# Performance work log

Measured on AMD Instinct MI355X. Metric: run time of the kernel, lower is better.

## Reference

```python
import jax, jax.numpy as jnp
import numpy as np

R = 3            # corr_radius
KK = 2 * R + 1   # 7
K = KK * KK      # 49 support points
LEVELS = 4       # corr_levels


def _offsets():
    # matches get_support_points: meshgrid over [-r, r] applied to (x, y)
    d = jnp.arange(-R, R + 1, dtype=jnp.float32)
    ox, oy = jnp.meshgrid(d, d, indexing='ij')
    return jnp.stack([ox, oy], -1).reshape(K, 2)


def _bilinear(fmap_flat, fidx, x, y):
    """Bilinear sample with zero padding (grid_sample align_corners=True semantics
    for pixel-space coords). fmap_flat: (F,H,W,D); fidx int (...); x,y float (...).
    Returns (..., D)."""
    Hs, Ws = fmap_flat.shape[1], fmap_flat.shape[2]
    x0 = jnp.floor(x); y0 = jnp.floor(y)
    tx = x - x0; ty = y - y0

    def tap(xi, yi, w):
        valid = (xi >= 0) & (xi <= Ws - 1) & (yi >= 0) & (yi <= Hs - 1)
        xc = jnp.clip(xi, 0, Ws - 1).astype(jnp.int32)
        yc = jnp.clip(yi, 0, Hs - 1).astype(jnp.int32)
        return fmap_flat[fidx, yc, xc] * (w * valid)[..., None]

    return (tap(x0, y0, (1 - tx) * (1 - ty)) + tap(x0 + 1, y0, tx * (1 - ty))
            + tap(x0, y0 + 1, (1 - tx) * ty) + tap(x0 + 1, y0 + 1, tx * ty))


def reference(fmaps, coords, queried_coords, queried_frames, w1, b1, w2, b2):
    """Multi-scale correlation-volume pipeline of CoTrackerThreeOffline:
    L2-normalize fmaps, build avg-pool pyramid, sample 7x7 track-support feats
    at query frames, sample 7x7 correlation feats at current coords per frame,
    einsum 49x49 corr volume, corr_mlp (2401->384 GELU ->256), concat levels."""
    B, T, D, H, W = fmaps.shape
    N = coords.shape[2]
    fm = jnp.transpose(fmaps, (0, 1, 3, 4, 2))  # (B,T,H,W,D)
    fm = fm / jnp.sqrt(jnp.maximum(jnp.sum(fm * fm, -1, keepdims=True), 1e-12))
    offs = _offsets()
    fidx_t = jnp.arange(B * T).reshape(B, T, 1, 1)          # frame index per (b,t)
    fq = (jnp.arange(B)[:, None] * T + queried_frames)[..., None]  # (B,N,1)
    embs = []
    for lvl in range(LEVELS):
        Hs, Ws = fm.shape[2], fm.shape[3]
        fm_flat = fm.reshape(B * T, Hs, Ws, D)
        # track support features at the query frame (7x7 around query coord)
        qc = queried_coords / (2.0 ** lvl)                   # (B,N,2)
        px = qc[..., 0:1] + offs[:, 0]; py = qc[..., 1:2] + offs[:, 1]  # (B,N,K)
        tf = _bilinear(fm_flat, fq, px, py)                  # (B,N,K,D)
        # correlation features around current coords for every frame
        cl = coords / (2.0 ** lvl)                           # (B,T,N,2)
        cx = cl[..., 0:1] + offs[:, 0]; cy = cl[..., 1:2] + offs[:, 1]  # (B,T,N,K)
        cf = _bilinear(fm_flat, fidx_t, cx, cy)              # (B,T,N,K,D)
        # 49x49 correlation volume then corr_mlp
        vol = jnp.einsum('btnkc,bnlc->btnkl', cf, tf).reshape(B * T * N, K * K)
        emb = jax.nn.gelu(vol @ w1 + b1, approximate=False) @ w2 + b2
        embs.append(emb.reshape(B, T, N, -1))
        if lvl < LEVELS - 1:  # avg_pool2d k=2 s=2
            fm = fm.reshape(B, T, Hs // 2, 2, Ws // 2, 2, D).mean(axis=(3, 5))
    return jnp.concatenate(embs, -1)  # (B,T,N,4*256)


def setup_inputs() -> dict:
    key = jax.random.key(0)
    ks = jax.random.split(key, 6)
    B, T, D, H, W, N = 1, 24, 128, 96, 128, 256
    fmaps = jax.random.normal(ks[0], (B, T, D, H, W), jnp.float32)
    scale_xy = jnp.array([W - 1.0, H - 1.0], jnp.float32)
    queried_coords = jax.random.uniform(ks[1], (B, N, 2), jnp.float32) * scale_xy
    queried_frames = jax.random.randint(ks[2], (B, N), 0, T)
    coords = jax.random.uniform(ks[3], (B, T, N, 2), jnp.float32) * scale_xy
    w1 = jax.random.normal(ks[4], (K * K, 384), jnp.float32) * 0.02
    b1 = jnp.zeros((384,), jnp.float32)
    w2 = jax.random.normal(ks[5], (384, 256), jnp.float32) * 0.02
    b2 = jnp.zeros((256,), jnp.float32)
    return dict(fmaps=fmaps, coords=coords, queried_coords=queried_coords,
                queried_frames=queried_frames, w1=w1, b1=b1, w2=w2, b2=b2)
```

## Files before the change

kernel.cpp:

```cpp
#include <hip/hip_runtime.h>
#include <hip/hip_bf16.h>
#include <stdint.h>

#define T_   24
#define D_   128
#define H_   96
#define W_   128
#define N_   256
#define KP   49
#define K2   3136
#define H1   384
#define OUTC 256
#define MTOT (4 * T_ * N_)

#define PAD  8

typedef __attribute__((ext_vector_type(8))) __bf16 bf16x8;
typedef __attribute__((ext_vector_type(4))) float f32x4;

typedef __attribute__((address_space(3))) unsigned int lds_u32;
typedef const __attribute__((address_space(1))) unsigned int g_u32;
#define GLOAD16(g, l) __builtin_amdgcn_global_load_lds((g_u32*)(g), (lds_u32*)(l), 16, 0, 0)

__device__ inline float bf2f(unsigned short u) {
    union { unsigned int i; float f; } v; v.i = ((unsigned int)u) << 16; return v.f;
}
__device__ inline unsigned short f2bf(float f) {
    union { float f; unsigned int i; } v; v.f = f;
    unsigned int i = v.i;
    return (unsigned short)((i + 0x7FFFu + ((i >> 16) & 1u)) >> 16);
}

__global__ __launch_bounds__(256) void k_padzero(uint4* __restrict__ fm,
                                                 int Hs, int Ws) {
    int PW = Ws + 2 * PAD, PH = Hs + 2 * PAD;
    size_t upf = (size_t)PH * PW * 16;
    size_t total = upf * T_;
    for (size_t idx = (size_t)blockIdx.x * 256 + threadIdx.x; idx < total;
         idx += (size_t)gridDim.x * 256) {
        size_t p = idx >> 4;
        size_t pf = p % ((size_t)PH * PW);
        int y = (int)(pf / PW), x = (int)(pf % PW);
        if (y < PAD || y >= Hs + PAD || x < PAD || x >= Ws + PAD) {
            uint4 z = {0u, 0u, 0u, 0u};
            fm[idx] = z;
        }
    }
}

__global__ __launch_bounds__(256) void k_w1t(const float* __restrict__ w1,
                                             unsigned short* __restrict__ w1t) {
    __shared__ float tile[64][65];
    int bn = blockIdx.x, k = blockIdx.y;
    int tid = threadIdx.x;
    int nl = tid & 63, q = tid >> 6;
#pragma unroll
    for (int i = 0; i < 16; ++i) {
        int l = q * 16 + i;
        float v = (l < KP) ? w1[((size_t)k * KP + l) * H1 + bn * 64 + nl] : 0.f;
        tile[l][nl] = v;
    }
    __syncthreads();
#pragma unroll
    for (int i = 0; i < 16; ++i) {
        int nn = q * 16 + i;
        w1t[(size_t)(bn * 64 + nn) * K2 + k * 64 + nl] = f2bf(tile[nl][nn]);
    }
}
__global__ __launch_bounds__(256) void k_w2t(const float* __restrict__ w2,
                                             unsigned short* __restrict__ w2t) {
    int idx = blockIdx.x * 256 + threadIdx.x;
    if (idx >= OUTC * H1) return;
    int j = idx / H1, k = idx % H1;
    w2t[idx] = f2bf(w2[(size_t)k * OUTC + j]);
}

#define PW0 (W_ + 2 * PAD)
#define FR0 ((size_t)(H_ + 2 * PAD) * PW0 * D_)
__global__ __launch_bounds__(256) void k_normalize(const float* __restrict__ fmaps,
                                                   unsigned short* __restrict__ fm0i) {
    int bid = blockIdx.x;
    int t = bid / H_, h = bid % H_;
    int tid = threadIdx.x;
    __shared__ float tile[64 * 129];
    __shared__ float ssumP[64][4];
    __shared__ float rs[64];
    const float* base = fmaps + (size_t)t * D_ * H_ * W_ + (size_t)h * W_;
    unsigned short* orow = fm0i + (size_t)t * FR0 + (size_t)h * (PW0 * D_);
    for (int wt = 0; wt < 2; ++wt) {
        int wl = tid & 63, dg = tid >> 6;
        float ss = 0.f;
        for (int i = 0; i < 32; ++i) {
            int d = dg * 32 + i;
            float v = base[(size_t)d * (H_ * W_) + wt * 64 + wl];
            tile[wl * 129 + d] = v;
            ss += v * v;
        }
        ssumP[wl][dg] = ss;
        __syncthreads();
        if (tid < 64)
            rs[tid] = rsqrtf(fmaxf(ssumP[tid][0] + ssumP[tid][1] + ssumP[tid][2] + ssumP[tid][3], 1e-12f));
        __syncthreads();
        int c = tid & 63, rg = tid >> 6;
        for (int i = 0; i < 16; ++i) {
            int wll = rg * 16 + i;
            float r = rs[wll];
            float v0 = tile[wll * 129 + c * 2] * r;
            float v1 = tile[wll * 129 + c * 2 + 1] * r;
            *(unsigned int*)(orow + (size_t)(wt * 64 + wll) * D_ + c * 2) =
                (unsigned int)f2bf(v0) | ((unsigned int)f2bf(v1) << 16);
        }
        __syncthreads();
    }
}

__global__ __launch_bounds__(256) void k_pool(const unsigned short* __restrict__ ini,
                                              unsigned short* __restrict__ outi,
                                              int Hs, int Ws) {
    int Ho = Hs >> 1, Wo = Ws >> 1;
    int PWi = Ws + 2 * PAD, PWo = Wo + 2 * PAD;
    size_t FRi = (size_t)(Hs + 2 * PAD) * PWi * D_;
    size_t FRo = (size_t)(Ho + 2 * PAD) * PWo * D_;
    size_t total = (size_t)T_ * Ho * Wo * (D_ / 4);
    size_t idx = (size_t)blockIdx.x * 256 + threadIdx.x;
    if (idx >= total) return;
    int d4 = idx & 31;
    size_t p = idx >> 5;
    int x = (int)(p % Wo); p /= Wo;
    int y = (int)(p % Ho); int t = (int)(p / Ho);
    const unsigned short* b0 = ini + (size_t)t * FRi + ((size_t)(2 * y) * PWi + 2 * x) * D_ + d4 * 4;
    const unsigned short* b1r = b0 + (size_t)PWi * D_;
    float acc[4] = {0.f, 0.f, 0.f, 0.f};
#pragma unroll
    for (int j = 0; j < 2; ++j) {
        const unsigned short* bb = j ? b1r : b0;
#pragma unroll
        for (int i = 0; i < 2; ++i) {
            const unsigned short* q = bb + i * D_;
#pragma unroll
            for (int c = 0; c < 4; ++c) acc[c] += bf2f(q[c]);
        }
    }
    unsigned short* o = outi + (size_t)t * FRo + ((size_t)y * PWo + x) * D_ + d4 * 4;
#pragma unroll
    for (int c = 0; c < 4; ++c) o[c] = f2bf(acc[c] * 0.25f);
}

__device__ inline float2 bilin2p(const unsigned short* __restrict__ fb, int PW,
                                 float px, float py, int lane) {
    float x0f = floorf(px), y0f = floorf(py);
    float tx = px - x0f, ty = py - y0f;
    int x0 = (int)x0f, y0 = (int)y0f;
    float acc0 = 0.f, acc1 = 0.f;
#pragma unroll
    for (int dy = 0; dy < 2; ++dy) {
#pragma unroll
        for (int dx = 0; dx < 2; ++dx) {
            long xi = x0 + dx, yi = y0 + dy;
            float w = (dx ? tx : 1.f - tx) * (dy ? ty : 1.f - ty);
            unsigned int pk = *(const unsigned int*)(fb + (yi * PW + xi) * D_ + lane * 2);
            acc0 += w * bf2f((unsigned short)(pk & 0xffffu));
            acc1 += w * bf2f((unsigned short)(pk >> 16));
        }
    }
    return {acc0, acc1};
}

__global__ __launch_bounds__(256) void k_tf(const unsigned short* __restrict__ f0,
                                            const unsigned short* __restrict__ f1,
                                            const unsigned short* __restrict__ f2,
                                            const unsigned short* __restrict__ f3,
                                            const float* __restrict__ qcoords,
                                            const int* __restrict__ qframes,
                                            unsigned short* __restrict__ tfg) {
    int n = blockIdx.x, lvl = blockIdx.y;
    const unsigned short* fmi = lvl == 0 ? f0 : lvl == 1 ? f1 : lvl == 2 ? f2 : f3;
    int Hs = H_ >> lvl, Ws = W_ >> lvl;
    int PW = Ws + 2 * PAD;
    size_t FR = (size_t)(Hs + 2 * PAD) * PW * D_;
    float inv = 1.0f / (float)(1 << lvl);
    int wid = threadIdx.x >> 6, lane = threadIdx.x & 63;
    int fidx = qframes[n];
    float qx = qcoords[n * 2 + 0] * inv, qy = qcoords[n * 2 + 1] * inv;
    const unsigned short* fb = fmi + (size_t)fidx * FR;
    unsigned short* orow = tfg + ((size_t)lvl * N_ + n) * (64 * D_);
    for (int k = wid; k < 64; k += 4) {
        float2 v = {0.f, 0.f};
        if (k < KP) {
            float px = qx + (float)(k / 7 - 3);
            float py = qy + (float)(k % 7 - 3);
            v = bilin2p(fb, PW, px, py, lane);
        }
        unsigned int pk = (unsigned int)f2bf(v.x) | ((unsigned int)f2bf(v.y) << 16);
        *(unsigned int*)(orow + k * D_ + lane * 2) = pk;
    }
}

__global__ __launch_bounds__(256) void k_cfvol(const unsigned short* __restrict__ f0,
                                               const unsigned short* __restrict__ f1,
                                               const unsigned short* __restrict__ f2,
                                               const unsigned short* __restrict__ f3,
                                               const float* __restrict__ coords,
                                               const unsigned short* __restrict__ tfg,
                                               unsigned short* __restrict__ vol) {
    __shared__ unsigned char tfs[16384];
    __shared__ unsigned char Ps[16384];
    unsigned short* Gs = (unsigned short*)tfs;
    int n = blockIdx.x, t = blockIdx.y, lvl = blockIdx.z;
    const unsigned short* fmi = lvl == 0 ? f0 : lvl == 1 ? f1 : lvl == 2 ? f2 : f3;
    int Hs = H_ >> lvl, Ws = W_ >> lvl;
    int PW = Ws + 2 * PAD;
    size_t FR = (size_t)(Hs + 2 * PAD) * PW * D_;
    float inv = 1.0f / (float)(1 << lvl);
    int tid = threadIdx.x, wid = tid >> 6, lane = tid & 63;
    int l15 = lane & 15, hi = lane >> 4;

    float cx = coords[((size_t)t * N_ + n) * 2 + 0] * inv;
    float cy = coords[((size_t)t * N_ + n) * 2 + 1] * inv;
    float fx = floorf(cx), fy = floorf(cy);
    float tx = cx - fx, ty = cy - fy;
    long bx = (long)(int)fx - 3, by = (long)(int)fy - 3;
    const unsigned short* fb = fmi + (size_t)t * FR;
    const unsigned short* tfn = tfg + ((size_t)lvl * N_ + n) * (64 * D_);
#pragma unroll
    for (int i = 0; i < 4; ++i) {
        int rr = wid * 16 + i * 4 + hi;
        int u = l15 ^ (rr & 7);
        GLOAD16(tfn + rr * 128 + u * 8, tfs + (wid * 4 + i) * 1024);
    }
#pragma unroll
    for (int i = 0; i < 4; ++i) {
        int rr = wid * 16 + i * 4 + hi;
        int u = l15 ^ (rr & 7);
        GLOAD16(fb + ((by + (rr & 7)) * (long)PW + (bx + (rr >> 3))) * D_ + u * 8,
                Ps + (wid * 4 + i) * 1024);
    }
    asm volatile("s_waitcnt vmcnt(0)" ::: "memory");
    __builtin_amdgcn_s_barrier();
    f32x4 acc[4] = {f32x4{0,0,0,0}, f32x4{0,0,0,0}, f32x4{0,0,0,0}, f32x4{0,0,0,0}};
#pragma unroll
    for (int ks = 0; ks < 4; ++ks) {
        int colb = ks * 64 + hi * 16;
        int arow = wid * 16 + l15;
        bf16x8 a = *(const bf16x8*)(Ps + arow * 256 + (colb ^ ((arow & 7) << 4)));
#pragma unroll
        for (int ln = 0; ln < 4; ++ln) {
            int brow = ln * 16 + l15;
            bf16x8 b = *(const bf16x8*)(tfs + brow * 256 + (colb ^ ((brow & 7) << 4)));
            acc[ln] = __builtin_amdgcn_mfma_f32_16x16x32_bf16(a, b, acc[ln], 0, 0, 0);
        }
    }
    __syncthreads();
#pragma unroll
    for (int ln = 0; ln < 4; ++ln)
#pragma unroll
        for (int r = 0; r < 4; ++r)
            Gs[(wid * 16 + hi * 4 + r) * 64 + ln * 16 + l15] = f2bf(acc[ln][r]);
    __syncthreads();
    unsigned int* vrow = (unsigned int*)(vol + (((size_t)lvl * T_ + t) * N_ + n) * K2);
    float w00 = (1.f - tx) * (1.f - ty), w01 = (1.f - tx) * ty;
    float w10 = tx * (1.f - ty), w11 = tx * ty;
    int lh = lane >> 5, ll = lane & 31;
#pragma unroll
    for (int it = 0; it < 7; ++it) {
        int k = it * 8 + wid * 2 + lh;
        if (k < KP) {
            int a0 = k / 7, b0 = k - a0 * 7;
            int g = a0 * 8 + b0;
            const unsigned short* gp = &Gs[g * 64 + ll * 2];
            unsigned int u00 = *(const unsigned int*)(gp);
            unsigned int u01 = *(const unsigned int*)(gp + 64);
            unsigned int u10 = *(const unsigned int*)(gp + 8 * 64);
            unsigned int u11 = *(const unsigned int*)(gp + 9 * 64);
            float r0 = w00 * bf2f((unsigned short)u00) + w01 * bf2f((unsigned short)u01)
                     + w10 * bf2f((unsigned short)u10) + w11 * bf2f((unsigned short)u11);
            float r1 = w00 * bf2f((unsigned short)(u00 >> 16)) + w01 * bf2f((unsigned short)(u01 >> 16))
                     + w10 * bf2f((unsigned short)(u10 >> 16)) + w11 * bf2f((unsigned short)(u11 >> 16));
            vrow[k * 32 + ll] = (unsigned int)f2bf(r0) | ((unsigned int)f2bf(r1) << 16);
        }
    }
}

__global__ __launch_bounds__(256) void k_gemm1(const unsigned short* __restrict__ A,
                                               const unsigned short* __restrict__ Bt,
                                               const float* __restrict__ b1,
                                               unsigned short* __restrict__ Hout) {
    __shared__ unsigned char As[8192];
    __shared__ unsigned char Bs[16384];
    int bid = blockIdx.x;
    int swz = (bid & 7) * 144 + (bid >> 3);
    int bm = swz / 3, bn = swz % 3;
    int tid = threadIdx.x, lane = tid & 63;
    int wid = tid >> 6, wm = wid & 1, wn = wid >> 1;
    int l15 = lane & 15, hi = lane >> 4;
    f32x4 acc[2][4] = {};
    const unsigned short* Abase = A + (size_t)(bm * 64) * K2;
    const unsigned short* Bbase = Bt + (size_t)(bn * 128) * K2;
    for (int kt = 0; kt < K2 / 64; ++kt) {
#pragma unroll
        for (int q = 0; q < 2; ++q) {
            int e = (wid * 2 + q) * 64 + lane;
            int row = e >> 3, su = (e & 7) ^ (row & 7);
            GLOAD16(Abase + (size_t)row * K2 + kt * 64 + su * 8, As + (wid * 2 + q) * 1024);
        }
#pragma unroll
        for (int q = 0; q < 4; ++q) {
            int e = (wid * 4 + q) * 64 + lane;
            int row = e >> 3, su = (e & 7) ^ (row & 7);
            GLOAD16(Bbase + (size_t)row * K2 + kt * 64 + su * 8, Bs + (wid * 4 + q) * 1024);
        }
        __syncthreads();
#pragma unroll
        for (int ks = 0; ks < 2; ++ks) {
            int colb = ks * 64 + hi * 16;
            bf16x8 a[2], b[4];
#pragma unroll
            for (int km = 0; km < 2; ++km) {
                int arow = wm * 32 + km * 16 + l15;
                a[km] = *(const bf16x8*)(As + arow * 128 + (colb ^ ((arow & 7) << 4)));
            }
#pragma unroll
            for (int ln = 0; ln < 4; ++ln) {
                int brow = wn * 64 + ln * 16 + l15;
                b[ln] = *(const bf16x8*)(Bs + brow * 128 + (colb ^ ((brow & 7) << 4)));
            }
#pragma unroll
            for (int km = 0; km < 2; ++km)
#pragma unroll
                for (int ln = 0; ln < 4; ++ln)
                    acc[km][ln] = __builtin_amdgcn_mfma_f32_16x16x32_bf16(a[km], b[ln], acc[km][ln], 0, 0, 0);
        }
        __syncthreads();
    }
#pragma unroll
    for (int km = 0; km < 2; ++km)
#pragma unroll
        for (int ln = 0; ln < 4; ++ln)
#pragma unroll
            for (int r = 0; r < 4; ++r) {
                int row = bm * 64 + wm * 32 + km * 16 + hi * 4 + r;
                int col = bn * 128 + wn * 64 + ln * 16 + l15;
                float x = acc[km][ln][r] + b1[col];
                float g = 0.5f * x * (1.f + erff(x * 0.70710678118654752f));
                Hout[(size_t)row * H1 + col] = f2bf(g);
            }
}

__global__ __launch_bounds__(256) void k_gemm2(const unsigned short* __restrict__ A,
                                               const unsigned short* __restrict__ Bt,
                                               const float* __restrict__ b2,
                                               float* __restrict__ outp) {
    __shared__ unsigned char As[8192];
    __shared__ unsigned char Bs[16384];
    int bid = blockIdx.x;
    int swz = (bid & 7) * 96 + (bid >> 3);
    int bm = swz >> 1, bn = swz & 1;
    int tid = threadIdx.x, lane = tid & 63;
    int wid = tid >> 6, wm = wid & 1, wn = wid >> 1;
    int l15 = lane & 15, hi = lane >> 4;
    f32x4 acc[2][4] = {};
    const unsigned short* Abase = A + (size_t)(bm * 64) * H1;
    const unsigned short* Bbase = Bt + (size_t)(bn * 128) * H1;
    for (int kt = 0; kt < H1 / 64; ++kt) {
#pragma unroll
        for (int q = 0; q < 2; ++q) {
            int e = (wid * 2 + q) * 64 + lane;
            int row = e >> 3, su = (e & 7) ^ (row & 7);
            GLOAD16(Abase + (size_t)row * H1 + kt * 64 + su * 8, As + (wid * 2 + q) * 1024);
        }
#pragma unroll
        for (int q = 0; q < 4; ++q) {
            int e = (wid * 4 + q) * 64 + lane;
            int row = e >> 3, su = (e & 7) ^ (row & 7);
            GLOAD16(Bbase + (size_t)row * H1 + kt * 64 + su * 8, Bs + (wid * 4 + q) * 1024);
        }
        __syncthreads();
#pragma unroll
        for (int ks = 0; ks < 2; ++ks) {
            int colb = ks * 64 + hi * 16;
            bf16x8 a[2], b[4];
#pragma unroll
            for (int km = 0; km < 2; ++km) {
                int arow = wm * 32 + km * 16 + l15;
                a[km] = *(const bf16x8*)(As + arow * 128 + (colb ^ ((arow & 7) << 4)));
            }
#pragma unroll
            for (int ln = 0; ln < 4; ++ln) {
                int brow = wn * 64 + ln * 16 + l15;
                b[ln] = *(const bf16x8*)(Bs + brow * 128 + (colb ^ ((brow & 7) << 4)));
            }
#pragma unroll
            for (int km = 0; km < 2; ++km)
#pragma unroll
                for (int ln = 0; ln < 4; ++ln)
                    acc[km][ln] = __builtin_amdgcn_mfma_f32_16x16x32_bf16(a[km], b[ln], acc[km][ln], 0, 0, 0);
        }
        __syncthreads();
    }
#pragma unroll
    for (int km = 0; km < 2; ++km)
#pragma unroll
        for (int ln = 0; ln < 4; ++ln)
#pragma unroll
            for (int r = 0; r < 4; ++r) {
                int row = bm * 64 + wm * 32 + km * 16 + hi * 4 + r;
                int col = bn * 128 + wn * 64 + ln * 16 + l15;
                int lvl = row / (T_ * N_);
                int r2 = row - lvl * (T_ * N_);
                outp[(size_t)r2 * (4 * OUTC) + lvl * OUTC + col] = acc[km][ln][r] + b2[col];
            }
}

extern "C" void kernel_launch(void* const* d_in, const int* in_sizes, int n_in,
                              void* d_out, int out_size, void* d_ws, size_t ws_size,
                              hipStream_t stream) {
    const float* fmaps   = (const float*)d_in[0];
    const float* coords  = (const float*)d_in[1];
    const float* qcoords = (const float*)d_in[2];
    const int*   qframes = (const int*)d_in[3];
    const float* w1      = (const float*)d_in[4];
    const float* b1      = (const float*)d_in[5];
    const float* w2      = (const float*)d_in[6];
    const float* b2      = (const float*)d_in[7];
    float* outp = (float*)d_out;

    unsigned char* ws = (unsigned char*)d_ws;
    size_t off = 0;
    auto take = [&](size_t bytes) {
        unsigned char* p = ws + off;
        off += (bytes + 255) & ~(size_t)255;
        return p;
    };
    const int Hs[4] = {96, 48, 24, 12}, Wss[4] = {128, 64, 32, 16};
    unsigned short* fmraw[4];
    unsigned short* fmint[4];
    for (int l = 0; l < 4; ++l) {
        int PH = Hs[l] + 2 * PAD, PW = Wss[l] + 2 * PAD;
        fmraw[l] = (unsigned short*)take((size_t)T_ * PH * PW * D_ * 2);
        fmint[l] = fmraw[l] + ((size_t)PAD * PW + PAD) * D_;
    }
    unsigned short* tfg  = (unsigned short*)take((size_t)4 * N_ * 64 * D_ * 2);
    unsigned short* vol  = (unsigned short*)take((size_t)MTOT * K2 * 2);
    unsigned short* hbuf = (unsigned short*)take((size_t)MTOT * H1 * 2);
    unsigned short* w1t  = (unsigned short*)take((size_t)H1 * K2 * 2);
    unsigned short* w2t  = (unsigned short*)take((size_t)OUTC * H1 * 2);

    for (int l = 0; l < 4; ++l)
        hipLaunchKernelGGL(k_padzero, dim3(4096), dim3(256), 0, stream,
                           (uint4*)fmraw[l], Hs[l], Wss[l]);
    hipLaunchKernelGGL(k_w1t, dim3(6, 49), dim3(256), 0, stream, w1, w1t);
    hipLaunchKernelGGL(k_w2t, dim3((OUTC * H1 + 255) / 256), dim3(256), 0, stream, w2, w2t);
    hipLaunchKernelGGL(k_normalize, dim3(T_ * H_), dim3(256), 0, stream, fmaps, fmint[0]);
    hipLaunchKernelGGL(k_pool, dim3((T_ * 48 * 64 * 32 + 255) / 256), dim3(256), 0, stream,
                       fmint[0], fmint[1], 96, 128);
    hipLaunchKernelGGL(k_pool, dim3((T_ * 24 * 32 * 32 + 255) / 256), dim3(256), 0, stream,
                       fmint[1], fmint[2], 48, 64);
    hipLaunchKernelGGL(k_pool, dim3((T_ * 12 * 16 * 32 + 255) / 256), dim3(256), 0, stream,
                       fmint[2], fmint[3], 24, 32);

    hipLaunchKernelGGL(k_tf, dim3(N_, 4), dim3(256), 0, stream,
                       fmint[0], fmint[1], fmint[2], fmint[3], qcoords, qframes, tfg);
    hipLaunchKernelGGL(k_cfvol, dim3(N_, T_, 4), dim3(256), 0, stream,
                       fmint[0], fmint[1], fmint[2], fmint[3], coords, tfg, vol);
    hipLaunchKernelGGL(k_gemm1, dim3(384 * 3), dim3(256), 0, stream, vol, w1t, b1, hbuf);
    hipLaunchKernelGGL(k_gemm2, dim3(384 * 2), dim3(256), 0, stream, hbuf, w2t, b2, outp);
}
```

Baseline: 324.8 us.

## Split-K the first MLP GEMM in two halves with separate bias+GELU reduction kernel

Pads the correlation-volume K dimension from 3136 to 3200 so it divides into two halves, and splits the first MLP GEMM into two K-halves, doubling the block count from 1152 to 2304. Each half writes fp32 partial sums to a new workspace. A separate kernel then sums the two partials, adds the bias, applies GELU and stores bf16. The aim is to fill the GPU better for the long-K GEMM. The cost is roughly 28 MB of extra fp32 partial traffic, one more launch, and a small amount of padded zero work.

New measurement: 354.3 us. 1.09x slower.

```diff
diff --git a/kernel.cpp b/kernel.cpp
--- a/kernel.cpp
+++ b/kernel.cpp
@@ -8,7 +8,7 @@
 #define W_   128
 #define N_   256
 #define KP   49
-#define K2   3136
+#define K2   3200
 #define H1   384
 #define OUTC 256
 #define MTOT (4 * T_ * N_)
@@ -57,7 +57,7 @@
 #pragma unroll
     for (int i = 0; i < 16; ++i) {
         int l = q * 16 + i;
-        float v = (l < KP) ? w1[((size_t)k * KP + l) * H1 + bn * 64 + nl] : 0.f;
+        float v = (k < KP && l < KP) ? w1[((size_t)k * KP + l) * H1 + bn * 64 + nl] : 0.f;
         tile[l][nl] = v;
     }
     __syncthreads();
@@ -279,24 +279,26 @@
             vrow[k * 32 + ll] = (unsigned int)f2bf(r0) | ((unsigned int)f2bf(r1) << 16);
         }
     }
-}
-
-__global__ __launch_bounds__(256) void k_gemm1(const unsigned short* __restrict__ A,
-                                               const unsigned short* __restrict__ Bt,
-                                               const float* __restrict__ b1,
-                                               unsigned short* __restrict__ Hout) {
+    if (tid < 32) vrow[1568 + tid] = 0u;
+}
+
+__global__ __launch_bounds__(256) void k_gemm1a(const unsigned short* __restrict__ A,
+                                                const unsigned short* __restrict__ Bt,
+                                                float* __restrict__ part) {
     __shared__ unsigned char As[8192];
     __shared__ unsigned char Bs[16384];
     int bid = blockIdx.x;
-    int swz = (bid & 7) * 144 + (bid >> 3);
-    int bm = swz / 3, bn = swz % 3;
+    int swz = (bid & 7) * 288 + (bid >> 3);
+    int tile = swz >> 1, kh = swz & 1;
+    int bm = tile / 3, bn = tile % 3;
     int tid = threadIdx.x, lane = tid & 63;
     int wid = tid >> 6, wm = wid & 1, wn = wid >> 1;
     int l15 = lane & 15, hi = lane >> 4;
     f32x4 acc[2][4] = {};
     const unsigned short* Abase = A + (size_t)(bm * 64) * K2;
     const unsigned short* Bbase = Bt + (size_t)(bn * 128) * K2;
-    for (int kt = 0; kt < K2 / 64; ++kt) {
+    const int KH = (K2 / 64) / 2;
+    for (int kt = kh * KH; kt < kh * KH + KH; ++kt) {
 #pragma unroll
         for (int q = 0; q < 2; ++q) {
             int e = (wid * 2 + q) * 64 + lane;
@@ -332,6 +334,7 @@
         }
         __syncthreads();
     }
+    float* pout = part + (size_t)kh * ((size_t)MTOT * H1);
 #pragma unroll
     for (int km = 0; km < 2; ++km)
 #pragma unroll
@@ -340,10 +343,26 @@
             for (int r = 0; r < 4; ++r) {
                 int row = bm * 64 + wm * 32 + km * 16 + hi * 4 + r;
                 int col = bn * 128 + wn * 64 + ln * 16 + l15;
-                float x = acc[km][ln][r] + b1[col];
-                float g = 0.5f * x * (1.f + erff(x * 0.70710678118654752f));
-                Hout[(size_t)row * H1 + col] = f2bf(g);
-            }
+                pout[(size_t)row * H1 + col] = acc[km][ln][r];
+            }
+}
+
+__global__ __launch_bounds__(256) void k_gfin(const float* __restrict__ part,
+                                              const float* __restrict__ b1,
+                                              unsigned short* __restrict__ Hout) {
+    size_t i2 = (size_t)blockIdx.x * 256 + threadIdx.x;
+    if (i2 >= (size_t)MTOT * H1 / 2) return;
+    size_t i = i2 * 2;
+    int col = (int)(i % H1);
+    size_t row = i / H1;
+    const float* p0 = part + row * H1 + col;
+    const float* p1 = p0 + (size_t)MTOT * H1;
+    float x0 = p0[0] + p1[0] + b1[col];
+    float x1 = p0[1] + p1[1] + b1[col + 1];
+    float g0 = 0.5f * x0 * (1.f + erff(x0 * 0.70710678118654752f));
+    float g1 = 0.5f * x1 * (1.f + erff(x1 * 0.70710678118654752f));
+    *(unsigned int*)(Hout + row * H1 + col) =
+        (unsigned int)f2bf(g0) | ((unsigned int)f2bf(g1) << 16);
 }
 
 __global__ __launch_bounds__(256) void k_gemm2(const unsigned short* __restrict__ A,
@@ -444,11 +463,12 @@
     unsigned short* hbuf = (unsigned short*)take((size_t)MTOT * H1 * 2);
     unsigned short* w1t  = (unsigned short*)take((size_t)H1 * K2 * 2);
     unsigned short* w2t  = (unsigned short*)take((size_t)OUTC * H1 * 2);
+    float*          part = (float*)take((size_t)2 * MTOT * H1 * 4);
 
     for (int l = 0; l < 4; ++l)
         hipLaunchKernelGGL(k_padzero, dim3(4096), dim3(256), 0, stream,
                            (uint4*)fmraw[l], Hs[l], Wss[l]);
-    hipLaunchKernelGGL(k_w1t, dim3(6, 49), dim3(256), 0, stream, w1, w1t);
+    hipLaunchKernelGGL(k_w1t, dim3(6, 50), dim3(256), 0, stream, w1, w1t);
     hipLaunchKernelGGL(k_w2t, dim3((OUTC * H1 + 255) / 256), dim3(256), 0, stream, w2, w2t);
     hipLaunchKernelGGL(k_normalize, dim3(T_ * H_), dim3(256), 0, stream, fmaps, fmint[0]);
     hipLaunchKernelGGL(k_pool, dim3((T_ * 48 * 64 * 32 + 255) / 256), dim3(256), 0, stream,
@@ -462,6 +482,8 @@
                        fmint[0], fmint[1], fmint[2], fmint[3], qcoords, qframes, tfg);
     hipLaunchKernelGGL(k_cfvol, dim3(N_, T_, 4), dim3(256), 0, stream,
                        fmint[0], fmint[1], fmint[2], fmint[3], coords, tfg, vol);
-    hipLaunchKernelGGL(k_gemm1, dim3(384 * 3), dim3(256), 0, stream, vol, w1t, b1, hbuf);
+    hipLaunchKernelGGL(k_gemm1a, dim3(2304), dim3(256), 0, stream, vol, w1t, part);
+    hipLaunchKernelGGL(k_gfin, dim3((int)(((size_t)MTOT * H1 / 2 + 255) / 256)), dim3(256),
+                       0, stream, part, b1, hbuf);
     hipLaunchKernelGGL(k_gemm2, dim3(384 * 2), dim3(256), 0, stream, hbuf, w2t, b2, outp);
 }
```
